# Kernel optimization log

Measured on AMD Instinct MI355X. Metric: run time of the kernel, lower is better.

Reference implementation:

```python
import jax, jax.numpy as jnp
import numpy as np

ROI_SIZES = (3, 7, 11)
IMAGE_SIZE = 960.0


def setup_inputs() -> dict:
    key = jax.random.key(0)
    ks = jax.random.split(key, 12)
    B, C, H, W = 1, 64, 120, 120
    N = 4096
    feature_maps = jax.random.normal(ks[0], (B, C, H, W), jnp.float32)
    cx = jax.random.uniform(ks[1], (N,), jnp.float32, 100.0, 860.0)
    cy = jax.random.uniform(ks[2], (N,), jnp.float32, 100.0, 860.0)
    bw = jax.random.uniform(ks[3], (N,), jnp.float32, 20.0, 240.0)
    bh = jax.random.uniform(ks[4], (N,), jnp.float32, 20.0, 240.0)
    boxes = jnp.stack([cx - bw / 2, cy - bh / 2, cx + bw / 2, cy + bh / 2], axis=1)
    s = 0.05
    w1 = jax.random.normal(ks[5], (64, 128), jnp.float32) * s
    b1 = jnp.zeros((128,), jnp.float32)
    w2 = jax.random.normal(ks[6], (128, 64), jnp.float32) * s
    b2 = jnp.zeros((64,), jnp.float32)
    p1 = jax.random.normal(ks[7], (256, 128), jnp.float32) * s
    pb1 = jnp.zeros((128,), jnp.float32)
    p2 = jax.random.normal(ks[8], (128, 64), jnp.float32) * s
    pb2 = jnp.zeros((64,), jnp.float32)
    return dict(feature_maps=feature_maps, boxes=boxes, w1=w1, b1=b1, w2=w2, b2=b2,
                p1=p1, pb1=pb1, p2=p2, pb2=pb2)


def _roi_pool(fm0, boxes_norm, r):
    """affine_grid + bilinear grid_sample (align_corners=False, zeros pad) + global avg pool.
    fm0: [C,H,W], boxes_norm: [N,4] in [-1,1]. Returns [N,C]."""
    C, H, W = fm0.shape
    x1, y1, x2, y2 = boxes_norm[:, 0], boxes_norm[:, 1], boxes_norm[:, 2], boxes_norm[:, 3]
    cx = (x1 + x2) / 2
    cy = (y1 + y2) / 2
    bw = jnp.clip(x2 - x1, 1e-6, None)
    bh = jnp.clip(y2 - y1, 1e-6, None)
    # affine_grid base coords with align_corners=False: (2i+1)/r - 1
    lin = (2.0 * jnp.arange(r, dtype=jnp.float32) + 1.0) / r - 1.0
    gx = cx[:, None, None] + (bw / 2)[:, None, None] * lin[None, None, :]  # [N,r,r]
    gy = cy[:, None, None] + (bh / 2)[:, None, None] * lin[None, :, None]  # [N,r,r]
    # normalized -> pixel coords (align_corners=False)
    ix = ((gx + 1.0) * W - 1.0) / 2.0
    iy = ((gy + 1.0) * H - 1.0) / 2.0
    x0f = jnp.floor(ix)
    y0f = jnp.floor(iy)
    wx1 = ix - x0f
    wy1 = iy - y0f
    x0 = x0f.astype(jnp.int32)
    y0 = y0f.astype(jnp.int32)
    fm_flat = fm0.reshape(C, H * W)

    def corner(xi, yi, wt):
        valid = (xi >= 0) & (xi < W) & (yi >= 0) & (yi < H)
        xi_c = jnp.clip(xi, 0, W - 1)
        yi_c = jnp.clip(yi, 0, H - 1)
        idx = yi_c * W + xi_c  # [N,r,r]
        vals = jnp.take(fm_flat, idx.reshape(-1), axis=1).reshape(C, *idx.shape)  # [C,N,r,r]
        return vals * (wt * valid.astype(wt.dtype))[None]

    out = (corner(x0, y0, (1 - wx1) * (1 - wy1))
           + corner(x0 + 1, y0, wx1 * (1 - wy1))
           + corner(x0, y0 + 1, (1 - wx1) * wy1)
           + corner(x0 + 1, y0 + 1, wx1 * wy1))
    return out.mean(axis=(2, 3)).T  # [N,C]


def _shared_head(x, w1, b1, w2, b2):
    h = jax.nn.relu(x @ w1 + b1)
    return jax.nn.relu(h @ w2 + b2)


def reference(feature_maps, boxes, w1, b1, w2, b2, p1, pb1, p2, pb2):
    B, C, H, W = feature_maps.shape
    N = boxes.shape[0]
    boxes_norm = boxes / IMAGE_SIZE * 2.0 - 1.0
    fm0 = feature_maps[0]
    feats = []
    for r in ROI_SIZES:
        pooled = _roi_pool(fm0, boxes_norm, r)  # [N,C]
        feats.append(_shared_head(pooled, w1, b1, w2, b2))
    # global context: avg-pool full map, expand to N
    g = feature_maps.mean(axis=(2, 3))  # [B,C], B=1
    g = jnp.broadcast_to(g, (N, C))
    feats.append(_shared_head(g, w1, b1, w2, b2))
    concat = jnp.concatenate(feats, axis=1)  # [N, 4*64]
    h = jax.nn.relu(concat @ p1 + pb1)
    return jax.nn.relu(h @ p2 + pb2)
```

## Files before the change

kernel.cpp:

```cpp
#include <hip/hip_runtime.h>
#include <hip/hip_bf16.h>


#define HW 120
#define NPIX (HW * HW)
#define TB 16

__global__ __launch_bounds__(256) void k_transpose_mean(
    const float* __restrict__ fm, float* __restrict__ fm_t,
    float* __restrict__ partial)
{
    __shared__ float tile[64][65];
    __shared__ float pr[4][64];
    const int t  = threadIdx.x;
    const int tx = t & 63;
    const int ty = t >> 6;
    const int pix0 = blockIdx.x * 64;

    #pragma unroll
    for (int k = 0; k < 16; ++k) {
        const int c = k * 4 + ty;
        tile[c][tx] = fm[c * NPIX + pix0 + tx];
    }
    __syncthreads();
    #pragma unroll
    for (int k = 0; k < 16; ++k) {
        const int p = k * 4 + ty;
        fm_t[(pix0 + p) * 64 + tx] = tile[tx][p];
    }
    float s = 0.f;
    #pragma unroll
    for (int k = 0; k < 16; ++k) s += tile[tx][ty * 16 + k];
    pr[ty][tx] = s;
    __syncthreads();
    if (t < 64)
        partial[blockIdx.x * 64 + t] = pr[0][t] + pr[1][t] + pr[2][t] + pr[3][t];
}

__global__ __launch_bounds__(256) void k_ghead(
    const float* __restrict__ partial,
    const float* __restrict__ w1, const float* __restrict__ b1,
    const float* __restrict__ w2, const float* __restrict__ b2,
    const float* __restrict__ p1, const float* __restrict__ pb1,
    float* __restrict__ f1pre)
{
    __shared__ float pr[4][64];
    __shared__ float g[64];
    __shared__ float h[128];
    __shared__ float gh[64];
    const int t = threadIdx.x;
    const int c = t & 63, q = t >> 6;
    float s = 0.f;
    for (int b = q; b < 225; b += 4) s += partial[b * 64 + c];
    pr[q][c] = s;
    __syncthreads();
    if (t < 64) g[t] = (pr[0][t] + pr[1][t] + pr[2][t] + pr[3][t]) * (1.f / 14400.f);
    __syncthreads();
    if (t < 128) {
        float a = b1[t];
        #pragma unroll 8
        for (int cc = 0; cc < 64; ++cc) a = fmaf(g[cc], w1[cc * 128 + t], a);
        h[t] = fmaxf(a, 0.f);
    }
    __syncthreads();
    if (t < 64) {
        float a = b2[t];
        #pragma unroll 8
        for (int k = 0; k < 128; ++k) a = fmaf(h[k], w2[k * 64 + t], a);
        gh[t] = fmaxf(a, 0.f);
    }
    __syncthreads();
    if (t < 128) {
        float a = pb1[t];
        #pragma unroll 8
        for (int j = 0; j < 64; ++j) a = fmaf(gh[j], p1[(192 + j) * 128 + t], a);
        f1pre[t] = a;
    }
}

__global__ __launch_bounds__(256) void k_pool(
    const float* __restrict__ fm_t, const float* __restrict__ boxes,
    float* __restrict__ pooled, int N)
{
    __shared__ int4   offL[4][192];
    __shared__ float4 wL[4][192];
    const int t    = threadIdx.x;
    const int lane = t & 63;
    const int wid  = t >> 6;
    const int n    = blockIdx.x * 4 + wid;
    if (n >= N) return;

    const float4 bx = reinterpret_cast<const float4*>(boxes)[n];
    const float x1 = bx.x / 960.f * 2.f - 1.f;
    const float y1 = bx.y / 960.f * 2.f - 1.f;
    const float x2 = bx.z / 960.f * 2.f - 1.f;
    const float y2 = bx.w / 960.f * 2.f - 1.f;
    const float cx  = (x1 + x2) * 0.5f;
    const float cy  = (y1 + y2) * 0.5f;
    const float bw2 = fmaxf(x2 - x1, 1e-6f) * 0.5f;
    const float bh2 = fmaxf(y2 - y1, 1e-6f) * 0.5f;

    #pragma unroll
    for (int rep = 0; rep < 3; ++rep) {
        const int p = lane + rep * 64;
        if (p < 179) {
            int i, j; float invR;
            if (p < 9)       { const int lp = p;      invR = 1.f / 3.f;  i = lp / 3;  j = lp - i * 3;  }
            else if (p < 58) { const int lp = p - 9;  invR = 1.f / 7.f;  i = lp / 7;  j = lp - i * 7;  }
            else             { const int lp = p - 58; invR = 1.f / 11.f; i = lp / 11; j = lp - i * 11; }
            const float liny = (float)(2 * i + 1) * invR - 1.f;
            const float linx = (float)(2 * j + 1) * invR - 1.f;
            const float gy = cy + bh2 * liny;
            const float gx = cx + bw2 * linx;
            const float iy = ((gy + 1.f) * 120.f - 1.f) * 0.5f;
            const float ix = ((gx + 1.f) * 120.f - 1.f) * 0.5f;
            const float y0f = floorf(iy), x0f = floorf(ix);
            const float wy = iy - y0f,  wx = ix - x0f;
            const int y0 = (int)y0f, x0 = (int)x0f;
            const float vy0 = (y0 >= 0 && y0 < HW)      ? 1.f : 0.f;
            const float vy1 = (y0 >= -1 && y0 < HW - 1) ? 1.f : 0.f;
            const float vx0 = (x0 >= 0 && x0 < HW)      ? 1.f : 0.f;
            const float vx1 = (x0 >= -1 && x0 < HW - 1) ? 1.f : 0.f;
            const float s2 = invR * invR;
            const int x0c = min(max(x0, 0), HW - 1);
            const int x1c = min(max(x0 + 1, 0), HW - 1);
            const int y0c = min(max(y0, 0), HW - 1);
            const int y1c = min(max(y0 + 1, 0), HW - 1);
            offL[wid][p] = make_int4((y0c * HW + x0c) * 64, (y0c * HW + x1c) * 64,
                                     (y1c * HW + x0c) * 64, (y1c * HW + x1c) * 64);
            wL[wid][p] = make_float4((1.f - wx) * (1.f - wy) * s2 * (vy0 * vx0),
                                     wx * (1.f - wy) * s2 * (vy0 * vx1),
                                     (1.f - wx) * wy * s2 * (vy1 * vx0),
                                     wx * wy * s2 * (vy1 * vx1));
        }
    }

    const float* lb = fm_t + lane;
    int p = 0;
    #pragma unroll
    for (int s = 0; s < 3; ++s) {
        const int pend = (s == 0) ? 9 : (s == 1 ? 58 : 179);
        float a0 = 0.f, a1 = 0.f, a2 = 0.f, a3 = 0.f;
        for (; p < pend; ++p) {
            const int4   o = offL[wid][p];
            const float4 w = wL[wid][p];
            a0 = fmaf(w.x, lb[o.x], a0);
            a1 = fmaf(w.y, lb[o.y], a1);
            a2 = fmaf(w.z, lb[o.z], a2);
            a3 = fmaf(w.w, lb[o.w], a3);
        }
        pooled[(s * N + n) * 64 + lane] = (a0 + a1) + (a2 + a3);
    }
}

__global__ __launch_bounds__(256) void k_heads(
    const float* __restrict__ pooled,
    const float* __restrict__ w1, const float* __restrict__ b1,
    const float* __restrict__ w2, const float* __restrict__ b2,
    const float* __restrict__ p1, const float* __restrict__ f1pre,
    const float* __restrict__ p2, const float* __restrict__ pb2,
    float* __restrict__ out, int N)
{
    __shared__ float X[3][TB][68];
    __shared__ float Hh[TB][132];
    __shared__ float cat[TB][196];
    __shared__ float F[TB][132];
    __shared__ float fp[128];

    const int t  = threadIdx.x;
    const int n0 = blockIdx.x * TB;

    for (int i = t; i < 3 * TB * 64; i += 256) {
        const int s = i >> 10;
        const int r = i & 1023;
        const int b = r >> 6;
        const int c = r & 63;
        const int n = n0 + b;
        X[s][b][c] = (n < N) ? pooled[(s * N + n) * 64 + c] : 0.f;
    }
    if (t < 128) fp[t] = f1pre[t];
    __syncthreads();

    const int k4  = t & 31;
    const int g8  = t >> 5;
    const int co4 = t & 15;
    const int g16 = t >> 4;
    const int ba = 2 * g8, bb = 2 * g8 + 1;

    #pragma unroll 1
    for (int s = 0; s < 3; ++s) {
        {
            const float4 bias = *reinterpret_cast<const float4*>(b1 + 4 * k4);
            float4 accA = bias, accB = bias;
            #pragma unroll 8
            for (int cc = 0; cc < 64; ++cc) {
                const float4 wv = *reinterpret_cast<const float4*>(w1 + cc * 128 + 4 * k4);
                const float xa = X[s][ba][cc], xb = X[s][bb][cc];
                accA.x = fmaf(xa, wv.x, accA.x); accA.y = fmaf(xa, wv.y, accA.y);
                accA.z = fmaf(xa, wv.z, accA.z); accA.w = fmaf(xa, wv.w, accA.w);
                accB.x = fmaf(xb, wv.x, accB.x); accB.y = fmaf(xb, wv.y, accB.y);
                accB.z = fmaf(xb, wv.z, accB.z); accB.w = fmaf(xb, wv.w, accB.w);
            }
            accA.x = fmaxf(accA.x, 0.f); accA.y = fmaxf(accA.y, 0.f);
            accA.z = fmaxf(accA.z, 0.f); accA.w = fmaxf(accA.w, 0.f);
            accB.x = fmaxf(accB.x, 0.f); accB.y = fmaxf(accB.y, 0.f);
            accB.z = fmaxf(accB.z, 0.f); accB.w = fmaxf(accB.w, 0.f);
            *reinterpret_cast<float4*>(&Hh[ba][4 * k4]) = accA;
            *reinterpret_cast<float4*>(&Hh[bb][4 * k4]) = accB;
        }
        __syncthreads();
        {
            const float4 bias = *reinterpret_cast<const float4*>(b2 + 4 * co4);
            float4 acc = bias;
            #pragma unroll 8
            for (int cc = 0; cc < 128; ++cc) {
                const float4 wv = *reinterpret_cast<const float4*>(w2 + cc * 64 + 4 * co4);
                const float h = Hh[g16][cc];
                acc.x = fmaf(h, wv.x, acc.x); acc.y = fmaf(h, wv.y, acc.y);
                acc.z = fmaf(h, wv.z, acc.z); acc.w = fmaf(h, wv.w, acc.w);
            }
            acc.x = fmaxf(acc.x, 0.f); acc.y = fmaxf(acc.y, 0.f);
            acc.z = fmaxf(acc.z, 0.f); acc.w = fmaxf(acc.w, 0.f);
            *reinterpret_cast<float4*>(&cat[g16][s * 64 + 4 * co4]) = acc;
        }
        __syncthreads();
    }

    {
        const float4 bias = *reinterpret_cast<const float4*>(fp + 4 * k4);
        float4 accA = bias, accB = bias;
        #pragma unroll 8
        for (int q = 0; q < 192; ++q) {
            const float4 wv = *reinterpret_cast<const float4*>(p1 + q * 128 + 4 * k4);
            const float xa = cat[ba][q], xb = cat[bb][q];
            accA.x = fmaf(xa, wv.x, accA.x); accA.y = fmaf(xa, wv.y, accA.y);
            accA.z = fmaf(xa, wv.z, accA.z); accA.w = fmaf(xa, wv.w, accA.w);
            accB.x = fmaf(xb, wv.x, accB.x); accB.y = fmaf(xb, wv.y, accB.y);
            accB.z = fmaf(xb, wv.z, accB.z); accB.w = fmaf(xb, wv.w, accB.w);
        }
        accA.x = fmaxf(accA.x, 0.f); accA.y = fmaxf(accA.y, 0.f);
        accA.z = fmaxf(accA.z, 0.f); accA.w = fmaxf(accA.w, 0.f);
        accB.x = fmaxf(accB.x, 0.f); accB.y = fmaxf(accB.y, 0.f);
        accB.z = fmaxf(accB.z, 0.f); accB.w = fmaxf(accB.w, 0.f);
        *reinterpret_cast<float4*>(&F[ba][4 * k4]) = accA;
        *reinterpret_cast<float4*>(&F[bb][4 * k4]) = accB;
    }
    __syncthreads();
    {
        const float4 bias = *reinterpret_cast<const float4*>(pb2 + 4 * co4);
        float4 acc = bias;
        #pragma unroll 8
        for (int cc = 0; cc < 128; ++cc) {
            const float4 wv = *reinterpret_cast<const float4*>(p2 + cc * 64 + 4 * co4);
            const float f = F[g16][cc];
            acc.x = fmaf(f, wv.x, acc.x); acc.y = fmaf(f, wv.y, acc.y);
            acc.z = fmaf(f, wv.z, acc.z); acc.w = fmaf(f, wv.w, acc.w);
        }
        acc.x = fmaxf(acc.x, 0.f); acc.y = fmaxf(acc.y, 0.f);
        acc.z = fmaxf(acc.z, 0.f); acc.w = fmaxf(acc.w, 0.f);
        const int n = n0 + g16;
        if (n < N)
            *reinterpret_cast<float4*>(out + n * 64 + 4 * co4) = acc;
    }
}

extern "C" void kernel_launch(void* const* d_in, const int* in_sizes, int n_in,
                              void* d_out, int out_size, void* d_ws, size_t ws_size,
                              hipStream_t stream)
{
    const float* fm    = (const float*)d_in[0];
    const float* boxes = (const float*)d_in[1];
    const float* w1    = (const float*)d_in[2];
    const float* b1    = (const float*)d_in[3];
    const float* w2    = (const float*)d_in[4];
    const float* b2    = (const float*)d_in[5];
    const float* p1    = (const float*)d_in[6];
    const float* pb1   = (const float*)d_in[7];
    const float* p2    = (const float*)d_in[8];
    const float* pb2   = (const float*)d_in[9];
    float* out = (float*)d_out;

    const int N = in_sizes[1] / 4;

    float* ws      = (float*)d_ws;
    float* fm_t    = ws;
    float* partial = fm_t + 921600;
    float* f1pre   = partial + 14400;
    float* pooled  = f1pre + 128;

    k_transpose_mean<<<NPIX / 64, 256, 0, stream>>>(fm, fm_t, partial);
    k_ghead<<<1, 256, 0, stream>>>(partial, w1, b1, w2, b2, p1, pb1, f1pre);
    k_pool<<<(N + 3) / 4, 256, 0, stream>>>(fm_t, boxes, pooled, N);
    k_heads<<<(N + TB - 1) / TB, 256, 0, stream>>>(pooled, w1, b1, w2, b2,
                                                   p1, f1pre, p2, pb2, out, N);
}
```

Before: 172.6 us.

## Fuse ROI pooling with MLP heads using per-wave readlane matvecs

Merges the pooling kernel and the head MLP kernel into one kernel. Each wavefront keeps its box's pooled features in registers and runs all four linear layers with wave-level readlane broadcasts, so the pooled intermediate never goes to global memory and one launch is removed. The cost is that each box now does matrix-vector work on its own, streaming every weight once per box instead of sharing weights across a tile of 16 boxes. That adds global/L2 weight traffic and serialised scalar readlane work, and the launch bounds now ask for 4 blocks per CU.

```diff
diff --git a/kernel.cpp b/kernel.cpp
--- a/kernel.cpp
+++ b/kernel.cpp
@@ -4,7 +4,10 @@
 
 #define HW 120
 #define NPIX (HW * HW)
-#define TB 16
+
+__device__ __forceinline__ float rdlane(float v, int l) {
+    return __int_as_float(__builtin_amdgcn_readlane(__float_as_int(v), l));
+}
 
 __global__ __launch_bounds__(256) void k_transpose_mean(
     const float* __restrict__ fm, float* __restrict__ fm_t,
@@ -78,9 +81,13 @@
     }
 }
 
-__global__ __launch_bounds__(256) void k_pool(
+__global__ __launch_bounds__(256, 4) void k_fused(
     const float* __restrict__ fm_t, const float* __restrict__ boxes,
-    float* __restrict__ pooled, int N)
+    const float* __restrict__ w1, const float* __restrict__ b1,
+    const float* __restrict__ w2, const float* __restrict__ b2,
+    const float* __restrict__ p1, const float* __restrict__ f1pre,
+    const float* __restrict__ p2, const float* __restrict__ pb2,
+    float* __restrict__ out, int N)
 {
     __shared__ int4   offL[4][192];
     __shared__ float4 wL[4][192];
@@ -136,131 +143,90 @@
     }
 
     const float* lb = fm_t + lane;
-    int p = 0;
-    #pragma unroll
-    for (int s = 0; s < 3; ++s) {
-        const int pend = (s == 0) ? 9 : (s == 1 ? 58 : 179);
-        float a0 = 0.f, a1 = 0.f, a2 = 0.f, a3 = 0.f;
-        for (; p < pend; ++p) {
-            const int4   o = offL[wid][p];
-            const float4 w = wL[wid][p];
-            a0 = fmaf(w.x, lb[o.x], a0);
-            a1 = fmaf(w.y, lb[o.y], a1);
-            a2 = fmaf(w.z, lb[o.z], a2);
-            a3 = fmaf(w.w, lb[o.w], a3);
-        }
-        pooled[(s * N + n) * 64 + lane] = (a0 + a1) + (a2 + a3);
-    }
-}
-
-__global__ __launch_bounds__(256) void k_heads(
-    const float* __restrict__ pooled,
-    const float* __restrict__ w1, const float* __restrict__ b1,
-    const float* __restrict__ w2, const float* __restrict__ b2,
-    const float* __restrict__ p1, const float* __restrict__ f1pre,
-    const float* __restrict__ p2, const float* __restrict__ pb2,
-    float* __restrict__ out, int N)
-{
-    __shared__ float X[3][TB][68];
-    __shared__ float Hh[TB][132];
-    __shared__ float cat[TB][196];
-    __shared__ float F[TB][132];
-    __shared__ float fp[128];
-
-    const int t  = threadIdx.x;
-    const int n0 = blockIdx.x * TB;
-
-    for (int i = t; i < 3 * TB * 64; i += 256) {
-        const int s = i >> 10;
-        const int r = i & 1023;
-        const int b = r >> 6;
-        const int c = r & 63;
-        const int n = n0 + b;
-        X[s][b][c] = (n < N) ? pooled[(s * N + n) * 64 + c] : 0.f;
-    }
-    if (t < 128) fp[t] = f1pre[t];
-    __syncthreads();
-
-    const int k4  = t & 31;
-    const int g8  = t >> 5;
-    const int co4 = t & 15;
-    const int g16 = t >> 4;
-    const int ba = 2 * g8, bb = 2 * g8 + 1;
-
-    #pragma unroll 1
-    for (int s = 0; s < 3; ++s) {
-        {
-            const float4 bias = *reinterpret_cast<const float4*>(b1 + 4 * k4);
-            float4 accA = bias, accB = bias;
-            #pragma unroll 8
-            for (int cc = 0; cc < 64; ++cc) {
-                const float4 wv = *reinterpret_cast<const float4*>(w1 + cc * 128 + 4 * k4);
-                const float xa = X[s][ba][cc], xb = X[s][bb][cc];
-                accA.x = fmaf(xa, wv.x, accA.x); accA.y = fmaf(xa, wv.y, accA.y);
-                accA.z = fmaf(xa, wv.z, accA.z); accA.w = fmaf(xa, wv.w, accA.w);
-                accB.x = fmaf(xb, wv.x, accB.x); accB.y = fmaf(xb, wv.y, accB.y);
-                accB.z = fmaf(xb, wv.z, accB.z); accB.w = fmaf(xb, wv.w, accB.w);
-            }
-            accA.x = fmaxf(accA.x, 0.f); accA.y = fmaxf(accA.y, 0.f);
-            accA.z = fmaxf(accA.z, 0.f); accA.w = fmaxf(accA.w, 0.f);
-            accB.x = fmaxf(accB.x, 0.f); accB.y = fmaxf(accB.y, 0.f);
-            accB.z = fmaxf(accB.z, 0.f); accB.w = fmaxf(accB.w, 0.f);
-            *reinterpret_cast<float4*>(&Hh[ba][4 * k4]) = accA;
-            *reinterpret_cast<float4*>(&Hh[bb][4 * k4]) = accB;
-        }
-        __syncthreads();
-        {
-            const float4 bias = *reinterpret_cast<const float4*>(b2 + 4 * co4);
-            float4 acc = bias;
-            #pragma unroll 8
-            for (int cc = 0; cc < 128; ++cc) {
-                const float4 wv = *reinterpret_cast<const float4*>(w2 + cc * 64 + 4 * co4);
-                const float h = Hh[g16][cc];
-                acc.x = fmaf(h, wv.x, acc.x); acc.y = fmaf(h, wv.y, acc.y);
-                acc.z = fmaf(h, wv.z, acc.z); acc.w = fmaf(h, wv.w, acc.w);
-            }
-            acc.x = fmaxf(acc.x, 0.f); acc.y = fmaxf(acc.y, 0.f);
-            acc.z = fmaxf(acc.z, 0.f); acc.w = fmaxf(acc.w, 0.f);
-            *reinterpret_cast<float4*>(&cat[g16][s * 64 + 4 * co4]) = acc;
-        }
-        __syncthreads();
-    }
-
-    {
-        const float4 bias = *reinterpret_cast<const float4*>(fp + 4 * k4);
-        float4 accA = bias, accB = bias;
-        #pragma unroll 8
-        for (int q = 0; q < 192; ++q) {
-            const float4 wv = *reinterpret_cast<const float4*>(p1 + q * 128 + 4 * k4);
-            const float xa = cat[ba][q], xb = cat[bb][q];
-            accA.x = fmaf(xa, wv.x, accA.x); accA.y = fmaf(xa, wv.y, accA.y);
-            accA.z = fmaf(xa, wv.z, accA.z); accA.w = fmaf(xa, wv.w, accA.w);
-            accB.x = fmaf(xb, wv.x, accB.x); accB.y = fmaf(xb, wv.y, accB.y);
-            accB.z = fmaf(xb, wv.z, accB.z); accB.w = fmaf(xb, wv.w, accB.w);
-        }
-        accA.x = fmaxf(accA.x, 0.f); accA.y = fmaxf(accA.y, 0.f);
-        accA.z = fmaxf(accA.z, 0.f); accA.w = fmaxf(accA.w, 0.f);
-        accB.x = fmaxf(accB.x, 0.f); accB.y = fmaxf(accB.y, 0.f);
-        accB.z = fmaxf(accB.z, 0.f); accB.w = fmaxf(accB.w, 0.f);
-        *reinterpret_cast<float4*>(&F[ba][4 * k4]) = accA;
-        *reinterpret_cast<float4*>(&F[bb][4 * k4]) = accB;
-    }
-    __syncthreads();
-    {
-        const float4 bias = *reinterpret_cast<const float4*>(pb2 + 4 * co4);
-        float4 acc = bias;
-        #pragma unroll 8
-        for (int cc = 0; cc < 128; ++cc) {
-            const float4 wv = *reinterpret_cast<const float4*>(p2 + cc * 64 + 4 * co4);
-            const float f = F[g16][cc];
-            acc.x = fmaf(f, wv.x, acc.x); acc.y = fmaf(f, wv.y, acc.y);
-            acc.z = fmaf(f, wv.z, acc.z); acc.w = fmaf(f, wv.w, acc.w);
-        }
-        acc.x = fmaxf(acc.x, 0.f); acc.y = fmaxf(acc.y, 0.f);
-        acc.z = fmaxf(acc.z, 0.f); acc.w = fmaxf(acc.w, 0.f);
-        const int n = n0 + g16;
-        if (n < N)
-            *reinterpret_cast<float4*>(out + n * 64 + 4 * co4) = acc;
+    float x0s, x1s, x2s;
+    {
+        float a0, a1, a2, a3;
+        #define GATHER(P0, P1, DST)                                        \
+        a0 = a1 = a2 = a3 = 0.f;                                           \
+        _Pragma("unroll 4")                                                \
+        for (int p = (P0); p < (P1); ++p) {                                \
+            const int4   o = offL[wid][p];                                 \
+            const float4 w = wL[wid][p];                                   \
+            a0 = fmaf(w.x, lb[o.x], a0);                                   \
+            a1 = fmaf(w.y, lb[o.y], a1);                                   \
+            a2 = fmaf(w.z, lb[o.z], a2);                                   \
+            a3 = fmaf(w.w, lb[o.w], a3);                                   \
+        }                                                                  \
+        DST = (a0 + a1) + (a2 + a3);
+        GATHER(0, 9, x0s)
+        GATHER(9, 58, x1s)
+        GATHER(58, 179, x2s)
+        #undef GATHER
+    }
+
+    float h0l, h0h, h1l, h1h, h2l, h2h;
+    {
+        const float bl = b1[lane], bh = b1[64 + lane];
+        h0l = bl; h0h = bh; h1l = bl; h1h = bh; h2l = bl; h2h = bh;
+        #pragma unroll 8
+        for (int cc = 0; cc < 64; ++cc) {
+            const float wlo = w1[cc * 128 + lane];
+            const float whi = w1[cc * 128 + 64 + lane];
+            const float xa0 = rdlane(x0s, cc);
+            const float xa1 = rdlane(x1s, cc);
+            const float xa2 = rdlane(x2s, cc);
+            h0l = fmaf(xa0, wlo, h0l); h0h = fmaf(xa0, whi, h0h);
+            h1l = fmaf(xa1, wlo, h1l); h1h = fmaf(xa1, whi, h1h);
+            h2l = fmaf(xa2, wlo, h2l); h2h = fmaf(xa2, whi, h2h);
+        }
+        h0l = fmaxf(h0l, 0.f); h0h = fmaxf(h0h, 0.f);
+        h1l = fmaxf(h1l, 0.f); h1h = fmaxf(h1h, 0.f);
+        h2l = fmaxf(h2l, 0.f); h2h = fmaxf(h2h, 0.f);
+    }
+
+    float c0, c1, c2;
+    {
+        const float bb = b2[lane];
+        c0 = bb; c1 = bb; c2 = bb;
+        #pragma unroll 8
+        for (int cc = 0; cc < 64; ++cc) {
+            const float wa = w2[cc * 64 + lane];
+            const float wb = w2[(cc + 64) * 64 + lane];
+            c0 = fmaf(rdlane(h0l, cc), wa, c0); c0 = fmaf(rdlane(h0h, cc), wb, c0);
+            c1 = fmaf(rdlane(h1l, cc), wa, c1); c1 = fmaf(rdlane(h1h, cc), wb, c1);
+            c2 = fmaf(rdlane(h2l, cc), wa, c2); c2 = fmaf(rdlane(h2h, cc), wb, c2);
+        }
+        c0 = fmaxf(c0, 0.f); c1 = fmaxf(c1, 0.f); c2 = fmaxf(c2, 0.f);
+    }
+
+    float flo = f1pre[lane], fhi = f1pre[64 + lane];
+    {
+        #define L3SEG(S, CREG)                                             \
+        _Pragma("unroll 8")                                                \
+        for (int j = 0; j < 64; ++j) {                                     \
+            const int q = (S) * 64 + j;                                    \
+            const float wlo = p1[q * 128 + lane];                          \
+            const float whi = p1[q * 128 + 64 + lane];                     \
+            const float xa = rdlane(CREG, j);                              \
+            flo = fmaf(xa, wlo, flo); fhi = fmaf(xa, whi, fhi);            \
+        }
+        L3SEG(0, c0)
+        L3SEG(1, c1)
+        L3SEG(2, c2)
+        #undef L3SEG
+        flo = fmaxf(flo, 0.f); fhi = fmaxf(fhi, 0.f);
+    }
+
+    {
+        float o = pb2[lane];
+        #pragma unroll 8
+        for (int j = 0; j < 64; ++j) {
+            const float wa = p2[j * 64 + lane];
+            const float wb = p2[(j + 64) * 64 + lane];
+            o = fmaf(rdlane(flo, j), wa, o);
+            o = fmaf(rdlane(fhi, j), wb, o);
+        }
+        out[n * 64 + lane] = fmaxf(o, 0.f);
     }
 }
 
@@ -286,11 +252,9 @@
     float* fm_t    = ws;
     float* partial = fm_t + 921600;
     float* f1pre   = partial + 14400;
-    float* pooled  = f1pre + 128;
 
     k_transpose_mean<<<NPIX / 64, 256, 0, stream>>>(fm, fm_t, partial);
     k_ghead<<<1, 256, 0, stream>>>(partial, w1, b1, w2, b2, p1, pb1, f1pre);
-    k_pool<<<(N + 3) / 4, 256, 0, stream>>>(fm_t, boxes, pooled, N);
-    k_heads<<<(N + TB - 1) / TB, 256, 0, stream>>>(pooled, w1, b1, w2, b2,
-                                                   p1, f1pre, p2, pb2, out, N);
-}
+    k_fused<<<(N + 3) / 4, 256, 0, stream>>>(fm_t, boxes, w1, b1, w2, b2,
+                                             p1, f1pre, p2, pb2, out, N);
+}
```

Result: faster. 160.1 us (-7.3%).
